# Kernel tuning notes

Measured on AMD Instinct MI355X. Metric: run time of the kernel, lower is better.

Reference implementation:

```python
import jax, jax.numpy as jnp
import numpy as np

H = 56; W = 56; WS = 7; SHIFT = 3; C = 256; NH = 8
HD = C // NH; N = WS * WS; NW = (H // WS) * (W // WS)
SCALE = HD ** -0.5
LN_EPS = 1e-5


def _rel_pos_index():
    coords = np.stack(np.meshgrid(np.arange(WS), np.arange(WS), indexing='ij'))  # (2, ws, ws)
    cf = coords.reshape(2, -1)
    rel = (cf[:, :, None] - cf[:, None, :]).transpose(1, 2, 0)  # (N, N, 2)
    rel[..., 0] += WS - 1
    rel[..., 1] += WS - 1
    rel[..., 0] *= 2 * WS - 1
    return rel.sum(-1)  # (N, N) indices into (2*ws-1)^2 table

RPI = jnp.asarray(_rel_pos_index())


def _attn_mask():
    img = np.zeros((H, W))
    slices = (slice(0, -WS), slice(-WS, -SHIFT), slice(-SHIFT, None))
    cnt = 0
    for hs in slices:
        for ws_ in slices:
            img[hs, ws_] = cnt
            cnt += 1
    mw = img.reshape(H // WS, WS, W // WS, WS).transpose(0, 2, 1, 3).reshape(-1, N)
    diff = mw[:, None, :] - mw[:, :, None]  # (nW, N, N), [w,i,j] = mw[w,j]-mw[w,i]
    return jnp.asarray(np.where(diff != 0, -100.0, 0.0).astype(np.float32))

AMASK = _attn_mask()  # (nW, N, N)


def ln(x, g, b):
    m = x.mean(-1, keepdims=True)
    v = x.var(-1, keepdims=True)
    return (x - m) / jnp.sqrt(v + LN_EPS) * g + b


def win_part(x):  # (B, H, W, C) -> (B*nW, N, C)
    B = x.shape[0]
    return x.reshape(B, H // WS, WS, W // WS, WS, C).transpose(0, 1, 3, 2, 4, 5).reshape(-1, N, C)


def win_rev(xw, B):  # (B*nW, N, C) -> (B, H, W, C)
    return xw.reshape(B, H // WS, W // WS, WS, WS, C).transpose(0, 1, 3, 2, 4, 5).reshape(B, H, W, C)


def setup_inputs() -> dict:
    key = jax.random.key(0)
    ks = iter(jax.random.split(key, 40))
    B, L = 16, H * W
    Ch = int(C * 4.0)
    p = {}
    p['x'] = jax.random.normal(next(ks), (B, L, C), jnp.float32)
    p['x_SAR'] = jax.random.normal(next(ks), (B, L, C), jnp.float32)
    p['ln1_g'] = jnp.ones((C,)); p['ln1_b'] = jnp.zeros((C,))
    p['ln1s_g'] = jnp.ones((C,)); p['ln1s_b'] = jnp.zeros((C,))
    p['qkv_w'] = jax.random.normal(next(ks), (3 * C, C)) * 0.02
    p['qkv_b'] = jnp.zeros((3 * C,))
    p['qkvs_w'] = jax.random.normal(next(ks), (3 * C, C)) * 0.02
    p['qkvs_b'] = jnp.zeros((3 * C,))
    p['rpb_table'] = jax.random.normal(next(ks), ((2 * WS - 1) ** 2, NH)) * 0.02
    p['fuse_w'] = jax.random.normal(next(ks), (NH, NH)) * 0.1  # Conv2d(8,8,1) weight squeezed
    p['fuse_b'] = jnp.zeros((NH,))
    p['proj_w'] = jax.random.normal(next(ks), (C, C)) * 0.02
    p['proj_b'] = jnp.zeros((C,))
    p['projs_w'] = jax.random.normal(next(ks), (C, C)) * 0.02
    p['projs_b'] = jnp.zeros((C,))
    p['ln2_g'] = jnp.ones((C,)); p['ln2_b'] = jnp.zeros((C,))
    p['ln2s_g'] = jnp.ones((C,)); p['ln2s_b'] = jnp.zeros((C,))
    p['fc1_w'] = jax.random.normal(next(ks), (Ch, C)) * 0.02
    p['fc1_b'] = jnp.zeros((Ch,))
    p['fc2_w'] = jax.random.normal(next(ks), (C, Ch)) * 0.02
    p['fc2_b'] = jnp.zeros((C,))
    p['fc1s_w'] = jax.random.normal(next(ks), (Ch, C)) * 0.02
    p['fc1s_b'] = jnp.zeros((Ch,))
    p['fc2s_w'] = jax.random.normal(next(ks), (C, Ch)) * 0.02
    p['fc2s_b'] = jnp.zeros((C,))
    return p


def reference(x, x_SAR, ln1_g, ln1_b, ln1s_g, ln1s_b, qkv_w, qkv_b, qkvs_w, qkvs_b,
              rpb_table, fuse_w, fuse_b, proj_w, proj_b, projs_w, projs_b,
              ln2_g, ln2_b, ln2s_g, ln2s_b, fc1_w, fc1_b, fc2_w, fc2_b,
              fc1s_w, fc1s_b, fc2s_w, fc2s_b):
    B = x.shape[0]
    sc, sc_s = x, x_SAR

    def pre(xx, g, b):  # norm -> spatial -> cyclic shift -> windows
        xs = ln(xx, g, b).reshape(B, H, W, C)
        xs = jnp.roll(xs, (-SHIFT, -SHIFT), axis=(1, 2))
        return win_part(xs)

    xw = pre(x, ln1_g, ln1_b)
    xws = pre(x_SAR, ln1s_g, ln1s_b)

    def qkv_f(xin, Wt, bt):
        qkv = (xin @ Wt.T + bt).reshape(-1, N, 3, NH, HD).transpose(2, 0, 3, 1, 4)
        return qkv[0], qkv[1], qkv[2]  # each (B*nW, nH, N, HD)

    q, k, v = qkv_f(xw, qkv_w, qkv_b)
    qs, ks_, vs = qkv_f(xws, qkvs_w, qkvs_b)

    attn = jnp.einsum('bhnd,bhmd->bhnm', q * SCALE, k)
    attn_s = jnp.einsum('bhnd,bhmd->bhnm', qs * SCALE, ks_)

    rpb = rpb_table[RPI.reshape(-1)].reshape(N, N, NH).transpose(2, 0, 1)  # (nH, N, N)
    attn = attn + rpb[None]
    attn_s = attn_s + rpb[None]

    # shift-window mask add
    attn = (attn.reshape(B, NW, NH, N, N) + AMASK[None, :, None]).reshape(-1, NH, N, N)
    attn_s = (attn_s.reshape(B, NW, NH, N, N) + AMASK[None, :, None]).reshape(-1, NH, N, N)

    # dual-branch fusion: 1x1 conv over head dim + sigmoid gate
    diff = attn_s - attn
    gate = jax.nn.sigmoid(jnp.einsum('oh,bhnm->bonm', fuse_w, diff) + fuse_b[None, :, None, None])
    attn_f = jax.nn.softmax(attn + diff * gate, axis=-1)
    attn_s = jax.nn.softmax(attn_s, axis=-1)

    def out_f(a, vv, pw, pb):
        o = jnp.einsum('bhnm,bhmd->bhnd', a, vv).transpose(0, 2, 1, 3).reshape(-1, N, C)
        return o @ pw.T + pb

    xo = out_f(attn_f, v, proj_w, proj_b)
    xos = out_f(attn_s, vs, projs_w, projs_b)

    def post(xout, scc, g2, b2, w1, b1, w2, b2m):
        xr = jnp.roll(win_rev(xout, B), (SHIFT, SHIFT), axis=(1, 2)).reshape(B, -1, C)
        xr = scc + xr
        h = jax.nn.gelu(ln(xr, g2, b2) @ w1.T + b1, approximate=False)
        return xr + (h @ w2.T + b2m)

    out = post(xo, sc, ln2_g, ln2_b, fc1_w, fc1_b, fc2_w, fc2_b)
    out_s = post(xos, sc_s, ln2s_g, ln2s_b, fc1s_w, fc1s_b, fc2s_w, fc2s_b)
    return out, out_s
```

## Files before the change

### kernel.cpp

```cpp
#include <hip/hip_runtime.h>
#include <hip/hip_bf16.h>
#include <cstdio>

typedef unsigned short ushort_t;
using bf16x8  = __attribute__((ext_vector_type(8))) __bf16;
using floatx4 = __attribute__((ext_vector_type(4))) float;

constexpr int    kTokens = 50176;
constexpr size_t TCsz    = (size_t)kTokens * 256;
constexpr float  kScale  = 0.17677669529663687f;
constexpr int    SPITCH  = 56;
constexpr size_t SPAIR   = 49 * 56;
constexpr size_t VTP     = 2048;
constexpr size_t VTSZ    = (size_t)8192 * VTP;

__device__ __forceinline__ float bf2f(ushort_t u) {
  unsigned int x = (unsigned int)u << 16;
  return __uint_as_float(x);
}
__device__ __forceinline__ ushort_t f2bf(float f) {
  __hip_bfloat16 h = __float2bfloat16(f);
  return *(ushort_t*)&h;
}

__device__ __forceinline__ void gl_lds16(const ushort_t* g, ushort_t* l) {
  __builtin_amdgcn_global_load_lds(
      (const __attribute__((address_space(1))) unsigned int*)g,
      (__attribute__((address_space(3))) unsigned int*)l, 16, 0, 0);
}

__global__ __launch_bounds__(256) void f2b_k(const float* __restrict__ src,
                                             ushort_t* __restrict__ dst, int n) {
  int i = blockIdx.x * 256 + threadIdx.x;
  if (i < n) dst[i] = f2bf(src[i]);
}

__global__ __launch_bounds__(256) void bias_k(const float* __restrict__ rpb,
                                              float* __restrict__ bias) {
  const int cls = blockIdx.x >> 3, head = blockIdx.x & 7;
  const int wh7 = cls >> 1, ww7 = cls & 1;
  float* bp = bias + (size_t)blockIdx.x * SPAIR;
  for (int e = threadIdx.x; e < (int)SPAIR; e += 256) {
    const int i = e / SPITCH, j = e % SPITCH;
    float val = 0.0f;
    if (j < 49) {
      const int yi = i / 7, xi = i % 7, yj = j / 7, xj = j % 7;
      val = rpb[((yi - yj + 6) * 13 + (xi - xj + 6)) * 8 + head];
      const int li = (wh7 ? (yi < 4 ? 1 : 2) : 0) * 3 + (ww7 ? (xi < 4 ? 1 : 2) : 0);
      const int lj = (wh7 ? (yj < 4 ? 1 : 2) : 0) * 3 + (ww7 ? (xj < 4 ? 1 : 2) : 0);
      if (li != lj) val -= 100.0f;
    }
    bp[e] = val;
  }
}

__global__ __launch_bounds__(256) void vtz_k(ushort_t* __restrict__ vtA,
                                             ushort_t* __restrict__ vtB) {
  const int id = blockIdx.x * 256 + threadIdx.x;
  ushort_t* base = (id < 262144) ? vtA : vtB;
  const size_t r = (size_t)(id & 262143) * 64;
  const uint4 z{0, 0, 0, 0};
  *(uint4*)(base + r + 48) = z;
  *(uint4*)(base + r + 56) = z;
}

template <int SHIFTED>
__global__ __launch_bounds__(256) void ln_k(const float* __restrict__ x,
                                            const float* __restrict__ g,
                                            const float* __restrict__ b,
                                            ushort_t* __restrict__ yout) {
  const int wave = threadIdx.x >> 6, lane = threadIdx.x & 63;
  const int t = blockIdx.x * 4 + wave;
  size_t src;
  if (SHIFTED) {
    int bb = t / 3136, r = t % 3136;
    int wi = r / 49, n = r % 49;
    int hp = (wi >> 3) * 7 + n / 7;
    int wp = (wi & 7) * 7 + n % 7;
    int sh = hp + 3; if (sh >= 56) sh -= 56;
    int sw = wp + 3; if (sw >= 56) sw -= 56;
    src = ((size_t)bb * 3136 + sh * 56 + sw) * 256;
  } else {
    src = (size_t)t * 256;
  }
  const float4 v4 = *(const float4*)(x + src + lane * 4);
  float s  = v4.x + v4.y + v4.z + v4.w;
  float s2 = v4.x * v4.x + v4.y * v4.y + v4.z * v4.z + v4.w * v4.w;
#pragma unroll
  for (int off = 32; off > 0; off >>= 1) {
    s  += __shfl_xor(s,  off);
    s2 += __shfl_xor(s2, off);
  }
  const float mean = s * (1.0f / 256.0f);
  const float var  = s2 * (1.0f / 256.0f) - mean * mean;
  const float rstd = rsqrtf(var + 1e-5f);
  const float4 g4 = *(const float4*)(g + lane * 4);
  const float4 b4 = *(const float4*)(b + lane * 4);
  ushort4 o;
  o.x = f2bf((v4.x - mean) * rstd * g4.x + b4.x);
  o.y = f2bf((v4.y - mean) * rstd * g4.y + b4.y);
  o.z = f2bf((v4.z - mean) * rstd * g4.z + b4.z);
  o.w = f2bf((v4.w - mean) * rstd * g4.w + b4.w);
  *(ushort4*)(yout + (size_t)t * 256 + lane * 4) = o;
}

template <int MODE>
__global__ __launch_bounds__(256) void bgemm_k(const ushort_t* __restrict__ A,
                                               const ushort_t* __restrict__ W,
                                               const float* __restrict__ bias,
                                               float* __restrict__ outf,
                                               ushort_t* __restrict__ outb,
                                               const float* __restrict__ aux,
                                               int K, int Nc) {
  __shared__ __align__(16) ushort_t As[128 * 32];
  __shared__ __align__(16) ushort_t Bs[128 * 32];
  const int tid = threadIdx.x;
  const int nbx = gridDim.x;
  const int nwg = nbx * gridDim.y;
  int flat = blockIdx.y * nbx + blockIdx.x;
  {
    const int xcd = flat & 7, idx = flat >> 3;
    const int q8 = nwg >> 3, r8 = nwg & 7;
    flat = (xcd < r8 ? xcd * (q8 + 1) : r8 * (q8 + 1) + (xcd - r8) * q8) + idx;
  }
  const int m0 = (flat / nbx) * 128;
  const int n0 = (flat % nbx) * 128;
  const int lane = tid & 63, wv = tid >> 6;
  const int wm = (wv >> 1) * 64, wn = (wv & 1) * 64;
  const int l16 = lane & 15, quad = lane >> 4;

  const int srow = tid >> 2;
  const int gkc  = (tid & 3) ^ ((tid >> 3) & 3);
  const ushort_t* Ag0 = A + (size_t)(m0 + srow) * K + gkc * 8;
  const ushort_t* Ag1 = A + (size_t)(m0 + 64 + srow) * K + gkc * 8;
  const ushort_t* Wg0 = W + (size_t)(n0 + srow) * K + gkc * 8;
  const ushort_t* Wg1 = W + (size_t)(n0 + 64 + srow) * K + gkc * 8;
  ushort_t* AsW0 = As + wv * 512;
  ushort_t* AsW1 = As + 2048 + wv * 512;
  ushort_t* BsW0 = Bs + wv * 512;
  ushort_t* BsW1 = Bs + 2048 + wv * 512;

  const int kcq = quad ^ ((l16 >> 1) & 3);
  const int arA = (wm + l16) * 32 + kcq * 8;
  const int arB = (wn + l16) * 32 + kcq * 8;

  floatx4 acc[4][4] = {};
  for (int k0 = 0; k0 < K; k0 += 32) {
    gl_lds16(Ag0, AsW0);
    gl_lds16(Ag1, AsW1);
    gl_lds16(Wg0, BsW0);
    gl_lds16(Wg1, BsW1);
    Ag0 += 32; Ag1 += 32; Wg0 += 32; Wg1 += 32;
    __syncthreads();
    bf16x8 af[4], bfr[4];
#pragma unroll
    for (int t = 0; t < 4; ++t) {
      af[t]  = *(const bf16x8*)&As[arA + t * 512];
      bfr[t] = *(const bf16x8*)&Bs[arB + t * 512];
    }
#pragma unroll
    for (int mt = 0; mt < 4; ++mt)
#pragma unroll
      for (int nt = 0; nt < 4; ++nt)
        acc[mt][nt] = __builtin_amdgcn_mfma_f32_16x16x32_bf16(af[mt], bfr[nt], acc[mt][nt], 0, 0, 0);
    __syncthreads();
  }

  if (MODE == 0) {
    int wis[16], ns[16];
#pragma unroll
    for (int mt = 0; mt < 4; ++mt) {
      int row = m0 + wm + mt * 16 + quad * 4;
      int wi = row / 49, n = row - wi * 49;
#pragma unroll
      for (int r = 0; r < 4; ++r) {
        wis[mt * 4 + r] = wi; ns[mt * 4 + r] = n;
        if (++n == 49) { n = 0; ++wi; }
      }
    }
    if (n0 < 512) {
      size_t rb[16];
#pragma unroll
      for (int i = 0; i < 16; ++i) rb[i] = (size_t)wis[i] * 12544 + (size_t)ns[i] * 32;
#pragma unroll
      for (int nt = 0; nt < 4; ++nt) {
        const int col = n0 + wn + nt * 16 + l16;
        const int which = col >> 8, head = (col >> 5) & 7, d = col & 31;
        const float bv = bias[col];
        const float sc = (which == 0) ? kScale : 1.0f;
        ushort_t* ob = outb + (size_t)which * TCsz + head * 1568 + d;
#pragma unroll
        for (int i = 0; i < 16; ++i)
          ob[rb[i]] = f2bf((acc[i >> 2][nt][i & 3] + bv) * sc);
      }
    } else {
      size_t rb[16];
#pragma unroll
      for (int i = 0; i < 16; ++i) rb[i] = (size_t)wis[i] * 16384 + (size_t)ns[i];
      ushort_t* vtb = (ushort_t*)outf;
#pragma unroll
      for (int nt = 0; nt < 4; ++nt) {
        const int col = n0 + wn + nt * 16 + l16;
        const int head = (col >> 5) & 7, d = col & 31;
        const float bv = bias[col];
        ushort_t* ob = vtb + head * 2048 + d * 64;
#pragma unroll
        for (int i = 0; i < 16; ++i)
          ob[rb[i]] = f2bf(acc[i >> 2][nt][i & 3] + bv);
      }
    }
  } else if (MODE == 1) {
    size_t rb[16];
#pragma unroll
    for (int mt = 0; mt < 4; ++mt) {
#pragma unroll
      for (int r = 0; r < 4; ++r) {
        const int row = m0 + wm + mt * 16 + quad * 4 + r;
        const int wi = row / 49, n = row - wi * 49;
        const int b = wi >> 6, wl = wi & 63;
        int h = (wl >> 3) * 7 + n / 7 + 3; if (h >= 56) h -= 56;
        int w = (wl & 7) * 7 + n % 7 + 3; if (w >= 56) w -= 56;
        rb[mt * 4 + r] = ((size_t)(b * 3136 + h * 56 + w)) * 256;
      }
    }
#pragma unroll
    for (int nt = 0; nt < 4; ++nt) {
      const int col = n0 + wn + nt * 16 + l16;
      const float bv = bias[col];
#pragma unroll
      for (int i = 0; i < 16; ++i) {
        const size_t idx = rb[i] + col;
        outf[idx] = aux[idx] + acc[i >> 2][nt][i & 3] + bv;
      }
    }
  } else if (MODE == 2) {
    size_t rb[16];
#pragma unroll
    for (int mt = 0; mt < 4; ++mt)
#pragma unroll
      for (int r = 0; r < 4; ++r)
        rb[mt * 4 + r] = (size_t)(m0 + wm + mt * 16 + quad * 4 + r) * Nc;
#pragma unroll
    for (int nt = 0; nt < 4; ++nt) {
      const int col = n0 + wn + nt * 16 + l16;
      const float bv = bias[col];
#pragma unroll
      for (int i = 0; i < 16; ++i) {
        float val = acc[i >> 2][nt][i & 3] + bv;
        val = 0.5f * val * (1.0f + erff(val * 0.70710678118654752f));
        outb[rb[i] + col] = f2bf(val);
      }
    }
  } else {
    size_t rb[16];
#pragma unroll
    for (int mt = 0; mt < 4; ++mt)
#pragma unroll
      for (int r = 0; r < 4; ++r)
        rb[mt * 4 + r] = (size_t)(m0 + wm + mt * 16 + quad * 4 + r) * 256;
#pragma unroll
    for (int nt = 0; nt < 4; ++nt) {
      const int col = n0 + wn + nt * 16 + l16;
      const float bv = bias[col];
#pragma unroll
      for (int i = 0; i < 16; ++i) {
        const size_t idx = rb[i] + col;
        outf[idx] = aux[idx] + acc[i >> 2][nt][i & 3] + bv;
      }
    }
  }
}

__global__ __launch_bounds__(256) void attn_k(const ushort_t* __restrict__ qA,
                                              const ushort_t* __restrict__ qB,
                                              const ushort_t* __restrict__ vtA,
                                              const ushort_t* __restrict__ vtB,
                                              const float* __restrict__ bias,
                                              const float* __restrict__ fw,
                                              const float* __restrict__ fb,
                                              ushort_t* __restrict__ Obase) {
  __shared__ __align__(16) ushort_t S[16 * 16 * 56 + 64];
  __shared__ float fwl[64], fbl[8];
  const int tid = threadIdx.x, lane = tid & 63, wv = tid >> 6;
  const int l16 = lane & 15, quad = lane >> 4;
  int bx = blockIdx.x;
  bx = (bx & 7) * 512 + (bx >> 3);
  const int win = bx >> 2, chunk = bx & 3;
  const int r0 = chunk * 16;
  const int rows = (r0 + 16 <= 49) ? 16 : (49 - r0);
  {
    uint4* p4 = (uint4*)S;
    for (int i = tid; i < 1800; i += 256) p4[i] = uint4{0, 0, 0, 0};
  }
  if (tid < 64) fwl[tid] = fw[tid];
  if (tid < 8)  fbl[tid] = fb[tid];
  __syncthreads();

  const int wl = win & 63;
  const int cls = (((wl >> 3) == 7) ? 2 : 0) + (((wl & 7) == 7) ? 1 : 0);

  const int qrow = (r0 + l16 <= 48) ? (r0 + l16) : 48;
  for (int i = 0; i < 4; ++i) {
    const int pair = wv * 4 + i;
    const int br = pair >> 3, h = pair & 7;
    const ushort_t* qb = (br ? qB : qA) + (size_t)(win * 8 + h) * 1568;
    const ushort_t* kb = qb + TCsz;
    const bf16x8 af = *(const bf16x8*)(qb + qrow * 32 + quad * 8);
    floatx4 acc[4];
#pragma unroll
    for (int nt = 0; nt < 4; ++nt) {
      const int krow = nt * 16 + l16;
      const int krc = (krow <= 48) ? krow : 48;
      const bf16x8 bfr = *(const bf16x8*)(kb + krc * 32 + quad * 8);
      acc[nt] = __builtin_amdgcn_mfma_f32_16x16x32_bf16(af, bfr, (floatx4){0.f, 0.f, 0.f, 0.f}, 0, 0, 0);
    }
    const float* bp = bias + (size_t)(cls * 8 + h) * SPAIR;
    ushort_t* Sp = S + pair * 896;
#pragma unroll
    for (int nt = 0; nt < 4; ++nt) {
      const int col = nt * 16 + l16;
      if (col >= SPITCH) continue;
#pragma unroll
      for (int r = 0; r < 4; ++r) {
        const int lrow = quad * 4 + r;
        if (lrow < rows)
          Sp[lrow * 56 + col] = (col < 49) ? f2bf(acc[nt][r] + bp[(r0 + lrow) * 56 + col]) : (ushort_t)0;
      }
    }
  }
  __syncthreads();

  const int np = rows * 49;
  for (int p = tid; p < np; p += 256) {
    const int lr = p / 49, c = p - lr * 49;
    const int off = lr * 56 + c;
    float sA[8], dd[8];
#pragma unroll
    for (int h = 0; h < 8; ++h) {
      sA[h] = bf2f(S[h * 896 + off]);
      dd[h] = bf2f(S[(8 + h) * 896 + off]) - sA[h];
    }
#pragma unroll
    for (int o = 0; o < 8; ++o) {
      float g = fbl[o];
#pragma unroll
      for (int h = 0; h < 8; ++h) g = fmaf(fwl[o * 8 + h], dd[h], g);
      g = __builtin_amdgcn_rcpf(1.0f + __expf(-g));
      S[o * 896 + off] = f2bf(sA[o] + dd[o] * g);
    }
  }
  __syncthreads();

  {
    const int lr = tid & 15, ph = tid >> 4;
    if (lr < rows) {
      ushort_t* row = S + ph * 896 + lr * 56;
      float mx = -1e30f;
      for (int m = 0; m < 49; ++m) mx = fmaxf(mx, bf2f(row[m]));
      float sum = 0.0f;
      for (int m = 0; m < 49; ++m) sum += __expf(bf2f(row[m]) - mx);
      const float inv = __builtin_amdgcn_rcpf(sum);
      for (int m = 0; m < 49; ++m) row[m] = f2bf(__expf(bf2f(row[m]) - mx) * inv);
    }
  }
  __syncthreads();

  for (int i = 0; i < 4; ++i) {
    const int pair = wv * 4 + i;
    const int br = pair >> 3, h = pair & 7;
    const ushort_t* vt = (br ? vtB : vtA) + (size_t)(win * 8 + h) * VTP;
    const ushort_t* Sp = S + pair * 896;
    floatx4 acc[2] = {};
#pragma unroll
    for (int ks = 0; ks < 2; ++ks) {
      const bf16x8 af = *(const bf16x8*)(Sp + l16 * 56 + ks * 32 + quad * 8);
#pragma unroll
      for (int nt = 0; nt < 2; ++nt) {
        const bf16x8 bv = *(const bf16x8*)(vt + (nt * 16 + l16) * 64 + ks * 32 + quad * 8);
        acc[nt] = __builtin_amdgcn_mfma_f32_16x16x32_bf16(af, bv, acc[nt], 0, 0, 0);
      }
    }
    ushort_t* Ob = Obase + (size_t)br * TCsz + (size_t)(win * 49 + r0) * 256 + h * 32;
#pragma unroll
    for (int nt = 0; nt < 2; ++nt)
#pragma unroll
      for (int r = 0; r < 4; ++r) {
        const int n = quad * 4 + r;
        if (n < rows) Ob[(size_t)n * 256 + nt * 16 + l16] = f2bf(acc[nt][r]);
      }
  }
}

extern "C" void kernel_launch(void* const* d_in, const int* in_sizes, int n_in,
                              void* d_out, int out_size, void* d_ws, size_t ws_size,
                              hipStream_t stream) {
  if (n_in < 29) { fprintf(stderr, "kernel_launch: expected 29 inputs, got %d\n", n_in); return; }
  const float* x      = (const float*)d_in[0];
  const float* xsar   = (const float*)d_in[1];
  const float* ln1_g  = (const float*)d_in[2];
  const float* ln1_b  = (const float*)d_in[3];
  const float* ln1s_g = (const float*)d_in[4];
  const float* ln1s_b = (const float*)d_in[5];
  const float* qkv_w  = (const float*)d_in[6];
  const float* qkv_b  = (const float*)d_in[7];
  const float* qkvs_w = (const float*)d_in[8];
  const float* qkvs_b = (const float*)d_in[9];
  const float* rpb    = (const float*)d_in[10];
  const float* fuse_w = (const float*)d_in[11];
  const float* fuse_b = (const float*)d_in[12];
  const float* proj_w = (const float*)d_in[13];
  const float* proj_b = (const float*)d_in[14];
  const float* projs_w = (const float*)d_in[15];
  const float* projs_b = (const float*)d_in[16];
  const float* ln2_g  = (const float*)d_in[17];
  const float* ln2_b  = (const float*)d_in[18];
  const float* ln2s_g = (const float*)d_in[19];
  const float* ln2s_b = (const float*)d_in[20];
  const float* fc1_w  = (const float*)d_in[21];
  const float* fc1_b  = (const float*)d_in[22];
  const float* fc2_w  = (const float*)d_in[23];
  const float* fc2_b  = (const float*)d_in[24];
  const float* fc1s_w = (const float*)d_in[25];
  const float* fc1s_b = (const float*)d_in[26];
  const float* fc2s_w = (const float*)d_in[27];
  const float* fc2s_b = (const float*)d_in[28];
  float* out = (float*)d_out;
  float* ws  = (float*)d_ws;

  const size_t need = 8 * TCsz * sizeof(float);
  if (ws_size < need) {
    fprintf(stderr, "kernel_launch: ws_size %zu < needed %zu\n", ws_size, need);
    return;
  }

  ushort_t* H   = (ushort_t*)ws;
  ushort_t* xw  = H;
  ushort_t* xws = H + TCsz;
  ushort_t* q   = H + 2 * TCsz;
  ushort_t* qs  = H + 5 * TCsz;
  ushort_t* vtA = H + 8 * TCsz;
  ushort_t* vtB = vtA + VTSZ;
  float* xr  = ws + 6 * TCsz;
  float* xrs = ws + 7 * TCsz;
  ushort_t* y   = H + 2 * TCsz;
  ushort_t* ysb = H + 3 * TCsz;
  ushort_t* hbuf = H + 4 * TCsz;
  ushort_t* wb  = H + 12 * TCsz - 1572864;
  float* biasbuf = (float*)(H + 12 * TCsz - 1572864 - 175616);
  ushort_t* wqkv  = wb;
  ushort_t* wqkvs = wb + 196608;
  ushort_t* wproj = wb + 393216;
  ushort_t* wprojs= wb + 458752;
  ushort_t* wfc1  = wb + 524288;
  ushort_t* wfc1s = wb + 786432;
  ushort_t* wfc2  = wb + 1048576;
  ushort_t* wfc2s = wb + 1310720;

  f2b_k<<<768, 256, 0, stream>>>(qkv_w,  wqkv,  196608);
  f2b_k<<<768, 256, 0, stream>>>(qkvs_w, wqkvs, 196608);
  f2b_k<<<256, 256, 0, stream>>>(proj_w, wproj, 65536);
  f2b_k<<<256, 256, 0, stream>>>(projs_w,wprojs,65536);
  f2b_k<<<1024,256, 0, stream>>>(fc1_w,  wfc1,  262144);
  f2b_k<<<1024,256, 0, stream>>>(fc1s_w, wfc1s, 262144);
  f2b_k<<<1024,256, 0, stream>>>(fc2_w,  wfc2,  262144);
  f2b_k<<<1024,256, 0, stream>>>(fc2s_w, wfc2s, 262144);
  bias_k<<<32, 256, 0, stream>>>(rpb, biasbuf);
  vtz_k<<<2048, 256, 0, stream>>>(vtA, vtB);

  ln_k<1><<<12544, 256, 0, stream>>>(x,    ln1_g,  ln1_b,  xw);
  ln_k<1><<<12544, 256, 0, stream>>>(xsar, ln1s_g, ln1s_b, xws);
  bgemm_k<0><<<dim3(6, 392), 256, 0, stream>>>(xw,  wqkv,  qkv_b,  (float*)vtA, q,  nullptr, 256, 768);
  bgemm_k<0><<<dim3(6, 392), 256, 0, stream>>>(xws, wqkvs, qkvs_b, (float*)vtB, qs, nullptr, 256, 768);
  attn_k<<<4096, 256, 0, stream>>>(q, qs, vtA, vtB, biasbuf, fuse_w, fuse_b, H);
  bgemm_k<1><<<dim3(2, 392), 256, 0, stream>>>(H,        wproj,  proj_b,  xr,  nullptr, x,    256, 256);
  bgemm_k<1><<<dim3(2, 392), 256, 0, stream>>>(H + TCsz, wprojs, projs_b, xrs, nullptr, xsar, 256, 256);
  ln_k<0><<<12544, 256, 0, stream>>>(xr,  ln2_g,  ln2_b,  y);
  ln_k<0><<<12544, 256, 0, stream>>>(xrs, ln2s_g, ln2s_b, ysb);
  bgemm_k<2><<<dim3(8, 392), 256, 0, stream>>>(y,    wfc1,  fc1_b,  nullptr, hbuf, nullptr, 256, 1024);
  bgemm_k<3><<<dim3(2, 392), 256, 0, stream>>>(hbuf, wfc2,  fc2_b,  out,     nullptr, xr,  1024, 256);
  bgemm_k<2><<<dim3(8, 392), 256, 0, stream>>>(ysb,  wfc1s, fc1s_b, nullptr, hbuf, nullptr, 256, 1024);
  bgemm_k<3><<<dim3(2, 392), 256, 0, stream>>>(hbuf, wfc2s, fc2s_b, out + TCsz, nullptr, xrs, 1024, 256);
}
```

Baseline: 970.4 us.

## Pre-lay bias in MFMA fragment order, vectorize softmax, defer normalization to PV output

The relative-position and mask bias table is rebuilt in MFMA accumulator fragment order, so each lane reads its 16 bias values with float4 loads instead of scattered scalar loads. The attention kernel now zeroes only the padding rows of shared memory rather than the whole buffer. Softmax rows are read and written as 8-wide bf16 vectors. The 1/sum normalization is moved out of the softmax pass and applied to the PV output via a small shared array. This cuts global and LDS traffic in the attention kernel, at the cost of a larger bias buffer and unnormalized bf16 probabilities feeding the PV MFMA.

```diff
diff --git a/kernel.cpp b/kernel.cpp
--- a/kernel.cpp
+++ b/kernel.cpp
@@ -4,13 +4,13 @@
 
 typedef unsigned short ushort_t;
 using bf16x8  = __attribute__((ext_vector_type(8))) __bf16;
+using u16x8   = __attribute__((ext_vector_type(8))) unsigned short;
 using floatx4 = __attribute__((ext_vector_type(4))) float;
 
 constexpr int    kTokens = 50176;
 constexpr size_t TCsz    = (size_t)kTokens * 256;
 constexpr float  kScale  = 0.17677669529663687f;
 constexpr int    SPITCH  = 56;
-constexpr size_t SPAIR   = 49 * 56;
 constexpr size_t VTP     = 2048;
 constexpr size_t VTSZ    = (size_t)8192 * VTP;
 
@@ -35,22 +35,29 @@
   if (i < n) dst[i] = f2bf(src[i]);
 }
 
-__global__ __launch_bounds__(256) void bias_k(const float* __restrict__ rpb,
-                                              float* __restrict__ bias) {
-  const int cls = blockIdx.x >> 3, head = blockIdx.x & 7;
+__global__ __launch_bounds__(64) void bias2_k(const float* __restrict__ rpb,
+                                              float* __restrict__ biasf) {
+  const int b = blockIdx.x;
+  const int head = b & 7, chunk = (b >> 3) & 3, cls = b >> 5;
   const int wh7 = cls >> 1, ww7 = cls & 1;
-  float* bp = bias + (size_t)blockIdx.x * SPAIR;
-  for (int e = threadIdx.x; e < (int)SPAIR; e += 256) {
-    const int i = e / SPITCH, j = e % SPITCH;
-    float val = 0.0f;
-    if (j < 49) {
-      const int yi = i / 7, xi = i % 7, yj = j / 7, xj = j % 7;
-      val = rpb[((yi - yj + 6) * 13 + (xi - xj + 6)) * 8 + head];
-      const int li = (wh7 ? (yi < 4 ? 1 : 2) : 0) * 3 + (ww7 ? (xi < 4 ? 1 : 2) : 0);
-      const int lj = (wh7 ? (yj < 4 ? 1 : 2) : 0) * 3 + (ww7 ? (xj < 4 ? 1 : 2) : 0);
-      if (li != lj) val -= 100.0f;
-    }
-    bp[e] = val;
+  const int lane = threadIdx.x;
+  float* bp = biasf + ((size_t)b * 64 + lane) * 16;
+#pragma unroll
+  for (int nt = 0; nt < 4; ++nt) {
+#pragma unroll
+    for (int r = 0; r < 4; ++r) {
+      const int row = chunk * 16 + (lane >> 4) * 4 + r;
+      const int col = nt * 16 + (lane & 15);
+      float val = 0.0f;
+      if (row < 49 && col < 49) {
+        const int yi = row / 7, xi = row % 7, yj = col / 7, xj = col % 7;
+        val = rpb[((yi - yj + 6) * 13 + (xi - xj + 6)) * 8 + head];
+        const int li = (wh7 ? (yi < 4 ? 1 : 2) : 0) * 3 + (ww7 ? (xi < 4 ? 1 : 2) : 0);
+        const int lj = (wh7 ? (yj < 4 ? 1 : 2) : 0) * 3 + (ww7 ? (xj < 4 ? 1 : 2) : 0);
+        if (li != lj) val -= 100.0f;
+      }
+      bp[nt * 4 + r] = val;
+    }
   }
 }
 
@@ -275,12 +282,13 @@
                                               const ushort_t* __restrict__ qB,
                                               const ushort_t* __restrict__ vtA,
                                               const ushort_t* __restrict__ vtB,
-                                              const float* __restrict__ bias,
+                                              const float* __restrict__ biasf,
                                               const float* __restrict__ fw,
                                               const float* __restrict__ fb,
                                               ushort_t* __restrict__ Obase) {
   __shared__ __align__(16) ushort_t S[16 * 16 * 56 + 64];
   __shared__ float fwl[64], fbl[8];
+  __shared__ float linv[256];
   const int tid = threadIdx.x, lane = tid & 63, wv = tid >> 6;
   const int l16 = lane & 15, quad = lane >> 4;
   int bx = blockIdx.x;
@@ -288,10 +296,15 @@
   const int win = bx >> 2, chunk = bx & 3;
   const int r0 = chunk * 16;
   const int rows = (r0 + 16 <= 49) ? 16 : (49 - r0);
-  {
-    uint4* p4 = (uint4*)S;
-    for (int i = tid; i < 1800; i += 256) p4[i] = uint4{0, 0, 0, 0};
-  }
+
+  if (rows < 16) {
+    const int per = (16 - rows) * 7;
+    for (int u = tid; u < 16 * per; u += 256) {
+      const int pr = u / per, off = u - pr * per;
+      *(uint4*)(S + pr * 896 + rows * 56 + off * 8) = uint4{0, 0, 0, 0};
+    }
+  }
+  if (tid < 16) *(uint4*)(S + 14336 + tid * 8) = uint4{0, 0, 0, 0};
   if (tid < 64) fwl[tid] = fw[tid];
   if (tid < 8)  fbl[tid] = fb[tid];
   __syncthreads();
@@ -314,17 +327,19 @@
       const bf16x8 bfr = *(const bf16x8*)(kb + krc * 32 + quad * 8);
       acc[nt] = __builtin_amdgcn_mfma_f32_16x16x32_bf16(af, bfr, (floatx4){0.f, 0.f, 0.f, 0.f}, 0, 0, 0);
     }
-    const float* bp = bias + (size_t)(cls * 8 + h) * SPAIR;
+    const float* bfp = biasf + ((size_t)((cls * 4 + chunk) * 8 + h) * 64 + lane) * 16;
     ushort_t* Sp = S + pair * 896;
 #pragma unroll
     for (int nt = 0; nt < 4; ++nt) {
       const int col = nt * 16 + l16;
       if (col >= SPITCH) continue;
+      const float4 bv4 = *(const float4*)(bfp + nt * 4);
+      const float bvv[4] = {bv4.x, bv4.y, bv4.z, bv4.w};
 #pragma unroll
       for (int r = 0; r < 4; ++r) {
         const int lrow = quad * 4 + r;
         if (lrow < rows)
-          Sp[lrow * 56 + col] = (col < 49) ? f2bf(acc[nt][r] + bp[(r0 + lrow) * 56 + col]) : (ushort_t)0;
+          Sp[lrow * 56 + col] = (col < 49) ? f2bf(acc[nt][r] + bvv[r]) : (ushort_t)0;
       }
     }
   }
@@ -355,12 +370,37 @@
     const int lr = tid & 15, ph = tid >> 4;
     if (lr < rows) {
       ushort_t* row = S + ph * 896 + lr * 56;
+      bf16x8 c[7];
+#pragma unroll
+      for (int j = 0; j < 7; ++j) c[j] = *(const bf16x8*)(row + j * 8);
       float mx = -1e30f;
-      for (int m = 0; m < 49; ++m) mx = fmaxf(mx, bf2f(row[m]));
+#pragma unroll
+      for (int j = 0; j < 6; ++j)
+#pragma unroll
+        for (int e = 0; e < 8; ++e) mx = fmaxf(mx, (float)c[j][e]);
+      mx = fmaxf(mx, (float)c[6][0]);
       float sum = 0.0f;
-      for (int m = 0; m < 49; ++m) sum += __expf(bf2f(row[m]) - mx);
-      const float inv = __builtin_amdgcn_rcpf(sum);
-      for (int m = 0; m < 49; ++m) row[m] = f2bf(__expf(bf2f(row[m]) - mx) * inv);
+#pragma unroll
+      for (int j = 0; j < 6; ++j) {
+        u16x8 o;
+#pragma unroll
+        for (int e = 0; e < 8; ++e) {
+          const float ev = __expf((float)c[j][e] - mx);
+          sum += ev;
+          o[e] = f2bf(ev);
+        }
+        *(u16x8*)(row + j * 8) = o;
+      }
+      {
+        const float ev = __expf((float)c[6][0] - mx);
+        sum += ev;
+        u16x8 o = {};
+        o[0] = f2bf(ev);
+        *(u16x8*)(row + 48) = o;
+      }
+      linv[tid] = __builtin_amdgcn_rcpf(sum);
+    } else {
+      linv[tid] = 1.0f;
     }
   }
   __syncthreads();
@@ -386,7 +426,8 @@
 #pragma unroll
       for (int r = 0; r < 4; ++r) {
         const int n = quad * 4 + r;
-        if (n < rows) Ob[(size_t)n * 256 + nt * 16 + l16] = f2bf(acc[nt][r]);
+        if (n < rows)
+          Ob[(size_t)n * 256 + nt * 16 + l16] = f2bf(acc[nt][r] * linv[pair * 16 + n]);
       }
   }
 }
@@ -446,7 +487,7 @@
   ushort_t* ysb = H + 3 * TCsz;
   ushort_t* hbuf = H + 4 * TCsz;
   ushort_t* wb  = H + 12 * TCsz - 1572864;
-  float* biasbuf = (float*)(H + 12 * TCsz - 1572864 - 175616);
+  float* biasf = (float*)(H + 12 * TCsz - 1572864 - 262144);
   ushort_t* wqkv  = wb;
   ushort_t* wqkvs = wb + 196608;
   ushort_t* wproj = wb + 393216;
@@ -464,14 +505,14 @@
   f2b_k<<<1024,256, 0, stream>>>(fc1s_w, wfc1s, 262144);
   f2b_k<<<1024,256, 0, stream>>>(fc2_w,  wfc2,  262144);
   f2b_k<<<1024,256, 0, stream>>>(fc2s_w, wfc2s, 262144);
-  bias_k<<<32, 256, 0, stream>>>(rpb, biasbuf);
+  bias2_k<<<128, 64, 0, stream>>>(rpb, biasf);
   vtz_k<<<2048, 256, 0, stream>>>(vtA, vtB);
 
   ln_k<1><<<12544, 256, 0, stream>>>(x,    ln1_g,  ln1_b,  xw);
   ln_k<1><<<12544, 256, 0, stream>>>(xsar, ln1s_g, ln1s_b, xws);
   bgemm_k<0><<<dim3(6, 392), 256, 0, stream>>>(xw,  wqkv,  qkv_b,  (float*)vtA, q,  nullptr, 256, 768);
   bgemm_k<0><<<dim3(6, 392), 256, 0, stream>>>(xws, wqkvs, qkvs_b, (float*)vtB, qs, nullptr, 256, 768);
-  attn_k<<<4096, 256, 0, stream>>>(q, qs, vtA, vtB, biasbuf, fuse_w, fuse_b, H);
+  attn_k<<<4096, 256, 0, stream>>>(q, qs, vtA, vtB, biasf, fuse_w, fuse_b, H);
   bgemm_k<1><<<dim3(2, 392), 256, 0, stream>>>(H,        wproj,  proj_b,  xr,  nullptr, x,    256, 256);
   bgemm_k<1><<<dim3(2, 392), 256, 0, stream>>>(H + TCsz, wprojs, projs_b, xrs, nullptr, xsar, 256, 256);
   ln_k<0><<<12544, 256, 0, stream>>>(xr,  ln2_g,  ln2_b,  y);
```

After: 937.9 us. 1.03x faster.
